# Kernel tuning notes

Measured on AMD Instinct MI355X. Metric: run time of the kernel, lower is better.

Reference implementation:

```python
import jax, jax.numpy as jnp
import numpy as np

D = 1024
H = 16
DH = D // H


def setup_inputs() -> dict:
    key = jax.random.key(0)
    ks = jax.random.split(key, 5)
    x = jax.random.normal(ks[0], (2, 2048, D), dtype=jnp.float32)
    s = 1.0 / np.sqrt(D)
    W_qkv = jax.random.normal(ks[1], (D, 3 * D), dtype=jnp.float32) * s
    b_qkv = jnp.zeros((3 * D,), dtype=jnp.float32)
    W_out = jax.random.normal(ks[2], (D, D), dtype=jnp.float32) * s
    b_out = jnp.zeros((D,), dtype=jnp.float32)
    return {"x": x, "W_qkv": W_qkv, "b_qkv": b_qkv, "W_out": W_out, "b_out": b_out}


def reference(x, W_qkv, b_qkv, W_out, b_out):
    B, N, _ = x.shape
    qkv = x @ W_qkv + b_qkv                       # [B,N,3D]
    qkv = qkv.reshape(B, N, 3, H, DH)
    q = jnp.transpose(qkv[:, :, 0], (0, 2, 1, 3))  # [B,H,N,DH]
    k = jnp.transpose(qkv[:, :, 1], (0, 2, 1, 3))
    v = jnp.transpose(qkv[:, :, 2], (0, 2, 1, 3))
    scores = jnp.einsum('bhnd,bhmd->bhnm', q, k) / jnp.sqrt(jnp.float32(DH))
    attn = jax.nn.softmax(scores, axis=-1)
    out = jnp.einsum('bhnm,bhmd->bhnd', attn, v)   # [B,H,N,DH]
    out = jnp.transpose(out, (0, 2, 1, 3)).reshape(B, N, D)
    return out @ W_out + b_out
```

## Files before the change

### kernel.cpp

```cpp
#include <hip/hip_runtime.h>

typedef unsigned short u16;
typedef unsigned int u32;
typedef __attribute__((ext_vector_type(8))) short bf16x8;
typedef __attribute__((ext_vector_type(4))) float f32x4;

static __device__ __forceinline__ void mfma16(f32x4& c, bf16x8 a, bf16x8 b) {
  asm("v_mfma_f32_16x16x32_bf16 %0, %1, %2, %0" : "+v"(c) : "v"(a), "v"(b));
}
static __device__ __forceinline__ float exp2_fast(float x) {
  float r; asm("v_exp_f32 %0, %1" : "=v"(r) : "v"(x)); return r;
}
static __device__ __forceinline__ u32 cvt_pk_bf16(float lo, float hi) {
  u32 r; asm("v_cvt_pk_bf16_f32 %0, %1, %2" : "=v"(r) : "v"(lo), "v"(hi)); return r;
}

static __device__ __forceinline__ float bfly_sum(float x) {
  x += __shfl_xor(x, 16);
  x += __shfl_xor(x, 32);
  return x;
}

static __device__ __forceinline__ u16 f2bf(float f) {
  union { float f; u32 u; } v; v.f = f;
  u32 r = v.u + 0x7fffu + ((v.u >> 16) & 1u);
  return (u16)(r >> 16);
}

typedef __attribute__((address_space(1))) void as1_v;
typedef __attribute__((address_space(3))) void as3_v;
static __device__ __forceinline__ void gload16(const u16* g, u16* l) {
  __builtin_amdgcn_global_load_lds((as1_v*)g, (as3_v*)l, 16, 0, 0);
}

__global__ __launch_bounds__(256) void cvt_bf16(const float* __restrict__ in,
                                                u16* __restrict__ out, int n4) {
  int i = blockIdx.x * 256 + threadIdx.x;
  if (i < n4) {
    float4 f = ((const float4*)in)[i];
    ushort4 u;
    u.x = f2bf(f.x); u.y = f2bf(f.y); u.z = f2bf(f.z); u.w = f2bf(f.w);
    ((ushort4*)out)[i] = u;
  }
}

__global__ __launch_bounds__(256) void transpose_cvt(const float* __restrict__ W,
                                                     u16* __restrict__ Wt,
                                                     int K, int Nc) {
  __shared__ float tile[32][33];
  int nb = blockIdx.x * 32, kb = blockIdx.y * 32;
  int tx = threadIdx.x, ty = threadIdx.y;
  for (int i = ty; i < 32; i += 8)
    tile[i][tx] = W[(size_t)(kb + i) * Nc + nb + tx];
  __syncthreads();
  for (int i = ty; i < 32; i += 8)
    Wt[(size_t)(nb + i) * K + kb + tx] = f2bf(tile[tx][i]);
}

__global__ __launch_bounds__(256) void vtrans(const u16* __restrict__ qkv,
                                              u16* __restrict__ vt) {
  __shared__ u16 t[64][72];
  const int tid = threadIdx.x;
  const int bh = blockIdx.y, nt = blockIdx.x;
  const int b = bh >> 4, h = bh & 15;
  const int n0 = nt * 64;
  const int r = tid >> 3, c = tid & 7;
  const u16* src = qkv + (size_t)(b * 2048 + n0 + r) * 3072 + 2048 + h * 64;
  *(int4*)&t[r][(c ^ ((r >> 3) & 7)) * 8] = *(const int4*)(src + c * 8);
  const u16* src2 = src + (size_t)32 * 3072;
  *(int4*)&t[r + 32][(c ^ (((r + 32) >> 3) & 7)) * 8] = *(const int4*)(src2 + c * 8);
  __syncthreads();
  const int d = tid >> 3, j0 = (tid & 7) * 8;
  union { int4 v; u16 u[8]; } o0, o1;
#pragma unroll
  for (int j = 0; j < 8; ++j) {
    const int row = j0 + j;
    const int sw = (row >> 3) & 7;
    o0.u[j] = t[row][((d >> 3) ^ sw) * 8 + (d & 7)];
    o1.u[j] = t[row][(((d + 32) >> 3) ^ sw) * 8 + ((d + 32) & 7)];
  }
  u16* dst = vt + (size_t)bh * 131072 + (size_t)d * 2048 + n0 + j0;
  *(int4*)dst = o0.v;
  *(int4*)(dst + (size_t)32 * 2048) = o1.v;
}

template <int OUT_F32>
__global__ __launch_bounds__(256) void gemm_bt(const u16* __restrict__ A,
                                               const u16* __restrict__ Bt,
                                               const float* __restrict__ bias,
                                               void* __restrict__ C,
                                               int M, int N, int K,
                                               float qscale, int qcols) {
  __shared__ u16 lA[2][4096];
  __shared__ u16 lB[2][4096];
  const int tid = threadIdx.x;
  const int lane = tid & 63, wid = tid >> 6;
  const int nbx = N >> 7;
  const int bx = blockIdx.x % nbx, by = blockIdx.x / nbx;
  const int m0 = by << 7, n0 = bx << 7;
  const int wr = wid >> 1, wc = wid & 1;

  const int srow = tid >> 2;
  const int scol = (tid & 3) << 3;
  const u16* gA0 = A + (size_t)(m0 + srow) * K + scol;
  const u16* gA1 = A + (size_t)(m0 + 64 + srow) * K + scol;
  const u16* gB0 = Bt + (size_t)(n0 + srow) * K + scol;
  const u16* gB1 = Bt + (size_t)(n0 + 64 + srow) * K + scol;

  const int rdA = (wr * 64 + (lane & 15)) * 32 + ((lane >> 4) * 8);
  const int rdB = (wc * 64 + (lane & 15)) * 32 + ((lane >> 4) * 8);

  f32x4 acc[4][4] = {};

  gload16(gA0, &lA[0][tid * 8]);
  gload16(gA1, &lA[0][2048 + tid * 8]);
  gload16(gB0, &lB[0][tid * 8]);
  gload16(gB1, &lB[0][2048 + tid * 8]);
  __syncthreads();

  const int nk = K >> 5;
  for (int t = 0; t < nk; ++t) {
    const int cur = t & 1, nxt = cur ^ 1;
    if (t + 1 < nk) {
      const int k0 = (t + 1) << 5;
      gload16(gA0 + k0, &lA[nxt][tid * 8]);
      gload16(gA1 + k0, &lA[nxt][2048 + tid * 8]);
      gload16(gB0 + k0, &lB[nxt][tid * 8]);
      gload16(gB1 + k0, &lB[nxt][2048 + tid * 8]);
    }
    bf16x8 aF[4], bF[4];
#pragma unroll
    for (int m = 0; m < 4; ++m) aF[m] = *(const bf16x8*)(&lA[cur][rdA + m * 512]);
#pragma unroll
    for (int n = 0; n < 4; ++n) bF[n] = *(const bf16x8*)(&lB[cur][rdB + n * 512]);
#pragma unroll
    for (int m = 0; m < 4; ++m)
#pragma unroll
      for (int n = 0; n < 4; ++n) mfma16(acc[m][n], aF[m], bF[n]);
    __syncthreads();
  }

#pragma unroll
  for (int n = 0; n < 4; ++n) {
    const int col = n0 + wc * 64 + n * 16 + (lane & 15);
    const float bv = bias[col];
    const float sc = (col < qcols) ? qscale : 1.0f;
#pragma unroll
    for (int m = 0; m < 4; ++m) {
      const int rbase = m0 + wr * 64 + m * 16 + ((lane >> 4) * 4);
#pragma unroll
      for (int r = 0; r < 4; ++r) {
        const float v = (acc[m][n][r] + bv) * sc;
        const size_t idx = (size_t)(rbase + r) * N + col;
        if (OUT_F32) ((float*)C)[idx] = v;
        else         ((u16*)C)[idx] = f2bf(v);
      }
    }
  }
}

__global__ __launch_bounds__(256) void attn_kernel(const u16* __restrict__ qkv,
                                                   const u16* __restrict__ vt,
                                                   u16* __restrict__ attn_out) {
  __shared__ u16 lK[2][4096];
  __shared__ u16 lV[2][4096];

  const int tid = threadIdx.x, lane = tid & 63, w = tid >> 6;
  const int l15 = lane & 15, g = lane >> 4;
  const int bid = blockIdx.x;
  const int tt = bid >> 3;
  const int qt = tt & 31;
  const int bh = ((tt >> 5) << 3) | (bid & 7);
  const int b = bh >> 4, h = bh & 15;

  const size_t rowQ = (size_t)(b * 2048 + qt * 64 + w * 16 + l15);
  const u16* qptr = qkv + rowQ * 3072 + h * 64 + g * 8;
  const bf16x8 qf0 = *(const bf16x8*)(qptr);
  const bf16x8 qf1 = *(const bf16x8*)(qptr + 32);

  const int r0 = tid >> 3, r1 = 32 + (tid >> 3);
  const int c0 = (tid & 7) ^ ((r0 ^ (r0 >> 3)) & 7);
  const int c1 = (tid & 7) ^ ((r1 ^ (r1 >> 3)) & 7);
  const u16* gk0 = qkv + (size_t)(b * 2048 + r0) * 3072 + 1024 + h * 64 + c0 * 8;
  const u16* gk1 = qkv + (size_t)(b * 2048 + r1) * 3072 + 1024 + h * 64 + c1 * 8;
  const u16* vtb = vt + (size_t)bh * 131072;
  const u16* gv0 = vtb + (size_t)r0 * 2048 + c0 * 8;
  const u16* gv1 = vtb + (size_t)r1 * 2048 + c1 * 8;

  int koff[4][2];
#pragma unroll
  for (int f = 0; f < 4; ++f) {
    const int R = 32 * (f >> 1) + 8 * (l15 >> 2) + 4 * ((l15 >> 1) & 1) +
                  2 * (f & 1) + (l15 & 1);
    const int sw = (R ^ (R >> 3)) & 7;
#pragma unroll
    for (int hf = 0; hf < 2; ++hf)
      koff[f][hf] = R * 64 + ((((hf << 2) | g) ^ sw) << 3);
  }
  int voff[4][2];
#pragma unroll
  for (int d = 0; d < 4; ++d) {
    const int R = d * 16 + l15;
    const int sw = (R ^ (R >> 3)) & 7;
#pragma unroll
    for (int kk = 0; kk < 2; ++kk)
      voff[d][kk] = R * 64 + ((((kk << 2) | g) ^ sw) << 3);
  }

  float lp = 0.f;
  f32x4 oacc[4] = {};

  gload16(gk0, &lK[0][tid * 8]);
  gload16(gk1, &lK[0][2048 + tid * 8]);
  gload16(gv0, &lV[0][tid * 8]);
  gload16(gv1, &lV[0][2048 + tid * 8]);
  __syncthreads();

  for (int it = 0; it < 32; ++it) {
    const int cur = it & 1, nxt = cur ^ 1;
    const u16* Kc = lK[cur];
    const u16* Vc = lV[cur];
    if (it + 1 < 32) {
      const size_t ko = (size_t)(it + 1) * 64 * 3072;
      const int vo = (it + 1) * 64;
      gload16(gk0 + ko, &lK[nxt][tid * 8]);
      gload16(gk1 + ko, &lK[nxt][2048 + tid * 8]);
      gload16(gv0 + vo, &lV[nxt][tid * 8]);
      gload16(gv1 + vo, &lV[nxt][2048 + tid * 8]);
    }

    f32x4 s[4] = {};
#pragma unroll
    for (int f = 0; f < 4; ++f) {
      mfma16(s[f], *(const bf16x8*)(Kc + koff[f][0]), qf0);
      mfma16(s[f], *(const bf16x8*)(Kc + koff[f][1]), qf1);
    }

#pragma unroll
    for (int f = 0; f < 4; ++f)
#pragma unroll
      for (int r = 0; r < 4; ++r) s[f][r] = exp2_fast(s[f][r]);
    lp += (((s[0][0] + s[0][1]) + (s[0][2] + s[0][3])) +
           ((s[1][0] + s[1][1]) + (s[1][2] + s[1][3]))) +
          (((s[2][0] + s[2][1]) + (s[2][2] + s[2][3])) +
           ((s[3][0] + s[3][1]) + (s[3][2] + s[3][3])));

    union { bf16x8 v; u32 u[4]; } p0, p1;
    p0.u[0] = cvt_pk_bf16(s[0][0], s[0][1]);
    p0.u[1] = cvt_pk_bf16(s[1][0], s[1][1]);
    p0.u[2] = cvt_pk_bf16(s[0][2], s[0][3]);
    p0.u[3] = cvt_pk_bf16(s[1][2], s[1][3]);
    p1.u[0] = cvt_pk_bf16(s[2][0], s[2][1]);
    p1.u[1] = cvt_pk_bf16(s[3][0], s[3][1]);
    p1.u[2] = cvt_pk_bf16(s[2][2], s[2][3]);
    p1.u[3] = cvt_pk_bf16(s[3][2], s[3][3]);

#pragma unroll
    for (int d = 0; d < 4; ++d) {
      mfma16(oacc[d], *(const bf16x8*)(Vc + voff[d][0]), p0.v);
      mfma16(oacc[d], *(const bf16x8*)(Vc + voff[d][1]), p1.v);
    }

    __syncthreads();
  }

  const float l_ = bfly_sum(lp);
  const float inv = 1.f / l_;
#pragma unroll
  for (int d = 0; d < 4; ++d)
#pragma unroll
    for (int r = 0; r < 4; ++r)
      attn_out[rowQ * 1024 + h * 64 + d * 16 + g * 4 + r] = f2bf(oacc[d][r] * inv);
}

extern "C" void kernel_launch(void* const* d_in, const int* in_sizes, int n_in,
                              void* d_out, int out_size, void* d_ws, size_t ws_size,
                              hipStream_t stream) {
  const float* x    = (const float*)d_in[0];
  const float* Wqkv = (const float*)d_in[1];
  const float* bqkv = (const float*)d_in[2];
  const float* Wout = (const float*)d_in[3];
  const float* bout = (const float*)d_in[4];
  float* out = (float*)d_out;

  char* ws = (char*)d_ws;
  u16* xb    = (u16*)(ws);
  u16* vt    = (u16*)(ws);
  u16* WqkvT = (u16*)(ws + 8388608);
  u16* WoutT = (u16*)(ws + 14680064);
  u16* qkvb  = (u16*)(ws + 16777216);
  u16* attnb = (u16*)(ws + 41943040);

  cvt_bf16<<<4096, 256, 0, stream>>>(x, xb, 4194304 / 4);
  transpose_cvt<<<dim3(96, 32), dim3(32, 8), 0, stream>>>(Wqkv, WqkvT, 1024, 3072);
  transpose_cvt<<<dim3(32, 32), dim3(32, 8), 0, stream>>>(Wout, WoutT, 1024, 1024);

  gemm_bt<0><<<dim3(24 * 32), 256, 0, stream>>>(xb, WqkvT, bqkv, qkvb,
                                                4096, 3072, 1024, 0.18033688f, 1024);
  vtrans<<<dim3(32, 32), 256, 0, stream>>>(qkvb, vt);
  attn_kernel<<<dim3(32 * 32), 256, 0, stream>>>(qkvb, vt, attnb);
  gemm_bt<1><<<dim3(8 * 32), 256, 0, stream>>>(attnb, WoutT, bout, out,
                                               4096, 1024, 1024, 1.0f, 0);
}
```

Measured before the change: 134.9 us.

## Switch attention kernel to 32x32 MFMA with 128-row query tiles

The attention kernel now uses v_mfma_f32_32x32x16_bf16, and each wave owns 32 query rows instead of 16, so a block covers 128 queries and the grid halves to 512 blocks. Each K/V tile loaded into LDS is reused across twice as many queries, which halves global and LDS traffic per query and needs fewer MFMA issues per FLOP. The P matrix is reassembled for the second MFMA with cross-half lane shuffles, and output stores are vectorized. The cost is more accumulator registers per thread and fewer blocks to spread across CUs.

```diff
diff --git a/kernel.cpp b/kernel.cpp
--- a/kernel.cpp
+++ b/kernel.cpp
@@ -3,22 +3,21 @@
 typedef unsigned short u16;
 typedef unsigned int u32;
 typedef __attribute__((ext_vector_type(8))) short bf16x8;
+typedef __attribute__((ext_vector_type(8))) __bf16 bf16v8;
 typedef __attribute__((ext_vector_type(4))) float f32x4;
+typedef __attribute__((ext_vector_type(16))) float f32x16;
 
 static __device__ __forceinline__ void mfma16(f32x4& c, bf16x8 a, bf16x8 b) {
   asm("v_mfma_f32_16x16x32_bf16 %0, %1, %2, %0" : "+v"(c) : "v"(a), "v"(b));
 }
+static __device__ __forceinline__ void mfma32(f32x16& c, bf16v8 a, bf16v8 b) {
+  c = __builtin_amdgcn_mfma_f32_32x32x16_bf16(a, b, c, 0, 0, 0);
+}
 static __device__ __forceinline__ float exp2_fast(float x) {
   float r; asm("v_exp_f32 %0, %1" : "=v"(r) : "v"(x)); return r;
 }
 static __device__ __forceinline__ u32 cvt_pk_bf16(float lo, float hi) {
   u32 r; asm("v_cvt_pk_bf16_f32 %0, %1, %2" : "=v"(r) : "v"(lo), "v"(hi)); return r;
-}
-
-static __device__ __forceinline__ float bfly_sum(float x) {
-  x += __shfl_xor(x, 16);
-  x += __shfl_xor(x, 32);
-  return x;
 }
 
 static __device__ __forceinline__ u16 f2bf(float f) {
@@ -166,17 +165,19 @@
   __shared__ u16 lV[2][4096];
 
   const int tid = threadIdx.x, lane = tid & 63, w = tid >> 6;
-  const int l15 = lane & 15, g = lane >> 4;
+  const int l31 = lane & 31, hi = lane >> 5;
   const int bid = blockIdx.x;
   const int tt = bid >> 3;
-  const int qt = tt & 31;
-  const int bh = ((tt >> 5) << 3) | (bid & 7);
+  const int qt = tt & 15;
+  const int bh = ((tt >> 4) << 3) | (bid & 7);
   const int b = bh >> 4, h = bh & 15;
 
-  const size_t rowQ = (size_t)(b * 2048 + qt * 64 + w * 16 + l15);
-  const u16* qptr = qkv + rowQ * 3072 + h * 64 + g * 8;
-  const bf16x8 qf0 = *(const bf16x8*)(qptr);
-  const bf16x8 qf1 = *(const bf16x8*)(qptr + 32);
+  const int qrow = b * 2048 + qt * 128 + w * 32 + l31;
+  const u16* qp = qkv + (size_t)qrow * 3072 + h * 64 + hi * 8;
+  const bf16v8 qB0 = *(const bf16v8*)(qp);
+  const bf16v8 qB1 = *(const bf16v8*)(qp + 16);
+  const bf16v8 qB2 = *(const bf16v8*)(qp + 32);
+  const bf16v8 qB3 = *(const bf16v8*)(qp + 48);
 
   const int r0 = tid >> 3, r1 = 32 + (tid >> 3);
   const int c0 = (tid & 7) ^ ((r0 ^ (r0 >> 3)) & 7);
@@ -187,28 +188,13 @@
   const u16* gv0 = vtb + (size_t)r0 * 2048 + c0 * 8;
   const u16* gv1 = vtb + (size_t)r1 * 2048 + c1 * 8;
 
-  int koff[4][2];
-#pragma unroll
-  for (int f = 0; f < 4; ++f) {
-    const int R = 32 * (f >> 1) + 8 * (l15 >> 2) + 4 * ((l15 >> 1) & 1) +
-                  2 * (f & 1) + (l15 & 1);
-    const int sw = (R ^ (R >> 3)) & 7;
-#pragma unroll
-    for (int hf = 0; hf < 2; ++hf)
-      koff[f][hf] = R * 64 + ((((hf << 2) | g) ^ sw) << 3);
-  }
-  int voff[4][2];
-#pragma unroll
-  for (int d = 0; d < 4; ++d) {
-    const int R = d * 16 + l15;
-    const int sw = (R ^ (R >> 3)) & 7;
-#pragma unroll
-    for (int kk = 0; kk < 2; ++kk)
-      voff[d][kk] = R * 64 + ((((kk << 2) | g) ^ sw) << 3);
-  }
+  const int sw0 = (l31 ^ (l31 >> 3)) & 7;
+  const int sw1 = ((32 + l31) ^ ((32 + l31) >> 3)) & 7;
+  const int base0 = l31 * 64;
+  const int base1 = (32 + l31) * 64;
 
   float lp = 0.f;
-  f32x4 oacc[4] = {};
+  f32x16 oacc0 = {}, oacc1 = {};
 
   gload16(gk0, &lK[0][tid * 8]);
   gload16(gk1, &lK[0][2048 + tid * 8]);
@@ -229,48 +215,92 @@
       gload16(gv1 + vo, &lV[nxt][2048 + tid * 8]);
     }
 
-    f32x4 s[4] = {};
-#pragma unroll
-    for (int f = 0; f < 4; ++f) {
-      mfma16(s[f], *(const bf16x8*)(Kc + koff[f][0]), qf0);
-      mfma16(s[f], *(const bf16x8*)(Kc + koff[f][1]), qf1);
-    }
-
-#pragma unroll
-    for (int f = 0; f < 4; ++f)
-#pragma unroll
-      for (int r = 0; r < 4; ++r) s[f][r] = exp2_fast(s[f][r]);
-    lp += (((s[0][0] + s[0][1]) + (s[0][2] + s[0][3])) +
-           ((s[1][0] + s[1][1]) + (s[1][2] + s[1][3]))) +
-          (((s[2][0] + s[2][1]) + (s[2][2] + s[2][3])) +
-           ((s[3][0] + s[3][1]) + (s[3][2] + s[3][3])));
-
-    union { bf16x8 v; u32 u[4]; } p0, p1;
-    p0.u[0] = cvt_pk_bf16(s[0][0], s[0][1]);
-    p0.u[1] = cvt_pk_bf16(s[1][0], s[1][1]);
-    p0.u[2] = cvt_pk_bf16(s[0][2], s[0][3]);
-    p0.u[3] = cvt_pk_bf16(s[1][2], s[1][3]);
-    p1.u[0] = cvt_pk_bf16(s[2][0], s[2][1]);
-    p1.u[1] = cvt_pk_bf16(s[3][0], s[3][1]);
-    p1.u[2] = cvt_pk_bf16(s[2][2], s[2][3]);
-    p1.u[3] = cvt_pk_bf16(s[3][2], s[3][3]);
-
-#pragma unroll
-    for (int d = 0; d < 4; ++d) {
-      mfma16(oacc[d], *(const bf16x8*)(Vc + voff[d][0]), p0.v);
-      mfma16(oacc[d], *(const bf16x8*)(Vc + voff[d][1]), p1.v);
-    }
+    f32x16 sA0 = {}, sA1 = {};
+    mfma32(sA0, *(const bf16v8*)(Kc + base0 + (((0 + hi) ^ sw0) << 3)), qB0);
+    mfma32(sA0, *(const bf16v8*)(Kc + base0 + (((2 + hi) ^ sw0) << 3)), qB1);
+    mfma32(sA0, *(const bf16v8*)(Kc + base0 + (((4 + hi) ^ sw0) << 3)), qB2);
+    mfma32(sA0, *(const bf16v8*)(Kc + base0 + (((6 + hi) ^ sw0) << 3)), qB3);
+    mfma32(sA1, *(const bf16v8*)(Kc + base1 + (((0 + hi) ^ sw1) << 3)), qB0);
+    mfma32(sA1, *(const bf16v8*)(Kc + base1 + (((2 + hi) ^ sw1) << 3)), qB1);
+    mfma32(sA1, *(const bf16v8*)(Kc + base1 + (((4 + hi) ^ sw1) << 3)), qB2);
+    mfma32(sA1, *(const bf16v8*)(Kc + base1 + (((6 + hi) ^ sw1) << 3)), qB3);
+
+#pragma unroll
+    for (int i = 0; i < 16; ++i) sA0[i] = exp2_fast(sA0[i]);
+#pragma unroll
+    for (int i = 0; i < 16; ++i) sA1[i] = exp2_fast(sA1[i]);
+    lp += (((sA0[0] + sA0[1]) + (sA0[2] + sA0[3])) +
+           ((sA0[4] + sA0[5]) + (sA0[6] + sA0[7]))) +
+          (((sA0[8] + sA0[9]) + (sA0[10] + sA0[11])) +
+           ((sA0[12] + sA0[13]) + (sA0[14] + sA0[15])));
+    lp += (((sA1[0] + sA1[1]) + (sA1[2] + sA1[3])) +
+           ((sA1[4] + sA1[5]) + (sA1[6] + sA1[7]))) +
+          (((sA1[8] + sA1[9]) + (sA1[10] + sA1[11])) +
+           ((sA1[12] + sA1[13]) + (sA1[14] + sA1[15])));
+
+    union { bf16v8 v; u32 u[4]; } pB0, pB1, pB2, pB3;
+    {
+      const u32 a01 = cvt_pk_bf16(sA0[0], sA0[1]), a23 = cvt_pk_bf16(sA0[2], sA0[3]);
+      const u32 b01 = cvt_pk_bf16(sA0[4], sA0[5]), b23 = cvt_pk_bf16(sA0[6], sA0[7]);
+      const u32 x01 = (u32)__shfl_xor((int)(hi ? a01 : b01), 32);
+      const u32 x23 = (u32)__shfl_xor((int)(hi ? a23 : b23), 32);
+      pB0.u[0] = hi ? x01 : a01;  pB0.u[1] = hi ? x23 : a23;
+      pB0.u[2] = hi ? b01 : x01;  pB0.u[3] = hi ? b23 : x23;
+    }
+    {
+      const u32 a01 = cvt_pk_bf16(sA0[8], sA0[9]), a23 = cvt_pk_bf16(sA0[10], sA0[11]);
+      const u32 b01 = cvt_pk_bf16(sA0[12], sA0[13]), b23 = cvt_pk_bf16(sA0[14], sA0[15]);
+      const u32 x01 = (u32)__shfl_xor((int)(hi ? a01 : b01), 32);
+      const u32 x23 = (u32)__shfl_xor((int)(hi ? a23 : b23), 32);
+      pB1.u[0] = hi ? x01 : a01;  pB1.u[1] = hi ? x23 : a23;
+      pB1.u[2] = hi ? b01 : x01;  pB1.u[3] = hi ? b23 : x23;
+    }
+    {
+      const u32 a01 = cvt_pk_bf16(sA1[0], sA1[1]), a23 = cvt_pk_bf16(sA1[2], sA1[3]);
+      const u32 b01 = cvt_pk_bf16(sA1[4], sA1[5]), b23 = cvt_pk_bf16(sA1[6], sA1[7]);
+      const u32 x01 = (u32)__shfl_xor((int)(hi ? a01 : b01), 32);
+      const u32 x23 = (u32)__shfl_xor((int)(hi ? a23 : b23), 32);
+      pB2.u[0] = hi ? x01 : a01;  pB2.u[1] = hi ? x23 : a23;
+      pB2.u[2] = hi ? b01 : x01;  pB2.u[3] = hi ? b23 : x23;
+    }
+    {
+      const u32 a01 = cvt_pk_bf16(sA1[8], sA1[9]), a23 = cvt_pk_bf16(sA1[10], sA1[11]);
+      const u32 b01 = cvt_pk_bf16(sA1[12], sA1[13]), b23 = cvt_pk_bf16(sA1[14], sA1[15]);
+      const u32 x01 = (u32)__shfl_xor((int)(hi ? a01 : b01), 32);
+      const u32 x23 = (u32)__shfl_xor((int)(hi ? a23 : b23), 32);
+      pB3.u[0] = hi ? x01 : a01;  pB3.u[1] = hi ? x23 : a23;
+      pB3.u[2] = hi ? b01 : x01;  pB3.u[3] = hi ? b23 : x23;
+    }
+
+    mfma32(oacc0, *(const bf16v8*)(Vc + base0 + (((0 + hi) ^ sw0) << 3)), pB0.v);
+    mfma32(oacc0, *(const bf16v8*)(Vc + base0 + (((2 + hi) ^ sw0) << 3)), pB1.v);
+    mfma32(oacc0, *(const bf16v8*)(Vc + base0 + (((4 + hi) ^ sw0) << 3)), pB2.v);
+    mfma32(oacc0, *(const bf16v8*)(Vc + base0 + (((6 + hi) ^ sw0) << 3)), pB3.v);
+    mfma32(oacc1, *(const bf16v8*)(Vc + base1 + (((0 + hi) ^ sw1) << 3)), pB0.v);
+    mfma32(oacc1, *(const bf16v8*)(Vc + base1 + (((2 + hi) ^ sw1) << 3)), pB1.v);
+    mfma32(oacc1, *(const bf16v8*)(Vc + base1 + (((4 + hi) ^ sw1) << 3)), pB2.v);
+    mfma32(oacc1, *(const bf16v8*)(Vc + base1 + (((6 + hi) ^ sw1) << 3)), pB3.v);
 
     __syncthreads();
   }
 
-  const float l_ = bfly_sum(lp);
-  const float inv = 1.f / l_;
-#pragma unroll
-  for (int d = 0; d < 4; ++d)
-#pragma unroll
-    for (int r = 0; r < 4; ++r)
-      attn_out[rowQ * 1024 + h * 64 + d * 16 + g * 4 + r] = f2bf(oacc[d][r] * inv);
+  lp += __shfl_xor(lp, 32);
+  const float inv = 1.f / lp;
+  u16* op = attn_out + (size_t)qrow * 1024 + h * 64 + hi * 4;
+#pragma unroll
+  for (int u = 0; u < 4; ++u) {
+    ushort4 o0, o1;
+    o0.x = f2bf(oacc0[4 * u + 0] * inv);
+    o0.y = f2bf(oacc0[4 * u + 1] * inv);
+    o0.z = f2bf(oacc0[4 * u + 2] * inv);
+    o0.w = f2bf(oacc0[4 * u + 3] * inv);
+    o1.x = f2bf(oacc1[4 * u + 0] * inv);
+    o1.y = f2bf(oacc1[4 * u + 1] * inv);
+    o1.z = f2bf(oacc1[4 * u + 2] * inv);
+    o1.w = f2bf(oacc1[4 * u + 3] * inv);
+    *(ushort4*)(op + 8 * u) = o0;
+    *(ushort4*)(op + 32 + 8 * u) = o1;
+  }
 }
 
 extern "C" void kernel_launch(void* const* d_in, const int* in_sizes, int n_in,
@@ -298,7 +328,7 @@
   gemm_bt<0><<<dim3(24 * 32), 256, 0, stream>>>(xb, WqkvT, bqkv, qkvb,
                                                 4096, 3072, 1024, 0.18033688f, 1024);
   vtrans<<<dim3(32, 32), 256, 0, stream>>>(qkvb, vt);
-  attn_kernel<<<dim3(32 * 32), 256, 0, stream>>>(qkvb, vt, attnb);
+  attn_kernel<<<dim3(512), 256, 0, stream>>>(qkvb, vt, attnb);
   gemm_bt<1><<<dim3(8 * 32), 256, 0, stream>>>(attnb, WoutT, bout, out,
                                                4096, 1024, 1024, 1.0f, 0);
 }
```

After: 141.0 us. +4.5%, slower.
